# Performance work log

Measured on AMD Instinct MI355X. Metric: run time of the kernel, lower is better.

## Reference

```python
import jax, jax.numpy as jnp
import numpy as np

HIDDEN = 1024
NUM_HEADS = 16
HEAD_DIM = HIDDEN // NUM_HEADS
MASK_BIAS = -10000.0


def setup_inputs() -> dict:
    key = jax.random.key(0)
    ks = jax.random.split(key, 5)
    B, S = 4, 2048
    hidden_states = jax.random.normal(ks[0], (B, S, HIDDEN), dtype=jnp.float32)
    # fused QKV projection (Linear1D_Col): hidden -> 3*hidden
    w_qkv = jax.random.normal(ks[1], (HIDDEN, 3 * HIDDEN), dtype=jnp.float32) * (HIDDEN ** -0.5)
    b_qkv = jax.random.normal(ks[2], (3 * HIDDEN,), dtype=jnp.float32) * 0.02
    # output dense (Linear1D_Row): hidden -> hidden
    w_dense = jax.random.normal(ks[3], (HIDDEN, HIDDEN), dtype=jnp.float32) * (HIDDEN ** -0.5)
    b_dense = jax.random.normal(ks[4], (HIDDEN,), dtype=jnp.float32) * 0.02
    return {"hidden_states": hidden_states, "w_qkv": w_qkv, "b_qkv": b_qkv,
            "w_dense": w_dense, "b_dense": b_dense}


def _split_heads(t):
    # [B, S, H*D] -> [B, H, S, D]
    B, S, _ = t.shape
    return t.reshape(B, S, NUM_HEADS, HEAD_DIM).transpose(0, 2, 1, 3)


def reference(hidden_states, w_qkv, b_qkv, w_dense, b_dense):
    B, S, _ = hidden_states.shape
    kvq = hidden_states @ w_qkv + b_qkv  # [B, S, 3*hidden]
    # NOTE: original chunk order is k, v, q (key first!)
    k, v, q = jnp.split(kvq, 3, axis=-1)
    q = _split_heads(q) * (HEAD_DIM ** -0.5)  # [B, H, S, D]
    k = _split_heads(k)
    v = _split_heads(v)
    scores = jnp.einsum('bhqd,bhkd->bhqk', q, k)  # [B, H, S, S]
    causal = jnp.tril(jnp.ones((S, S), dtype=bool))
    scores = jnp.where(causal[None, None], scores, jnp.asarray(MASK_BIAS, scores.dtype))
    dt = scores.dtype
    attn = jax.nn.softmax(scores.astype(jnp.float32), axis=-1).astype(dt)
    ctx = jnp.einsum('bhqk,bhkd->bhqd', attn, v)  # [B, H, S, D]
    ctx = ctx.transpose(0, 2, 1, 3).reshape(B, S, HIDDEN)
    return ctx @ w_dense + b_dense
```

## Files before the change

kernel.cpp:

```cpp
#include <hip/hip_runtime.h>

#define H_NUM 16
#define HD    64
#define SQ    2048
#define HID   1024
#define MTOK  8192

typedef __attribute__((ext_vector_type(8))) short bf16x8;
typedef __attribute__((ext_vector_type(4))) short s16x4;
typedef __attribute__((ext_vector_type(4))) float f32x4;

__device__ __forceinline__ short f2bf(float f) {
  union { float f; unsigned u; } v; v.f = f;
  unsigned r = v.u + 0x7fffu + ((v.u >> 16) & 1u);
  return (short)(r >> 16);
}

__device__ __forceinline__ float fexp2(float x) {
#if __has_builtin(__builtin_amdgcn_exp2f)
  return __builtin_amdgcn_exp2f(x);
#else
  return exp2f(x);
#endif
}

__device__ __forceinline__ void gload_lds16(const short* g, short* l) {
  __builtin_amdgcn_global_load_lds(
      (const __attribute__((address_space(1))) void*)g,
      (__attribute__((address_space(3))) void*)l, 16, 0, 0);
}

__global__ void k_cvt(const float* __restrict__ in, short* __restrict__ out, int n4) {
  int i = blockIdx.x * blockDim.x + threadIdx.x;
  if (i < n4) {
    float4 f = ((const float4*)in)[i];
    s16x4 o = { f2bf(f.x), f2bf(f.y), f2bf(f.z), f2bf(f.w) };
    ((s16x4*)out)[i] = o;
  }
}

__global__ void k_tr(const float* __restrict__ in, short* __restrict__ out, int R, int C) {
  __shared__ float t[32][33];
  int c0 = blockIdx.x * 32, r0 = blockIdx.y * 32;
  int tx = threadIdx.x, ty = threadIdx.y;
#pragma unroll
  for (int i = 0; i < 4; i++)
    t[ty + 8 * i][tx] = in[(size_t)(r0 + ty + 8 * i) * C + c0 + tx];
  __syncthreads();
#pragma unroll
  for (int i = 0; i < 4; i++)
    out[(size_t)(c0 + ty + 8 * i) * R + r0 + tx] = f2bf(t[tx][ty + 8 * i]);
}

template <int EPI>
__global__ __launch_bounds__(256) void k_gemm(
    const short* __restrict__ A, const short* __restrict__ Bt,
    const float* __restrict__ bias,
    short* __restrict__ qbuf, short* __restrict__ kbuf, short* __restrict__ vtbuf,
    float* __restrict__ outf, int Kd) {
  __shared__ short as[128][64];
  __shared__ short bs[128][64];
  const int tid = threadIdx.x;
  const int w = tid >> 6, l = tid & 63;
  const int lr = l & 15, lk = l >> 4;
  const int wr = w >> 1, wc = w & 1;
  const int nwg = gridDim.x * gridDim.y;
  const int lin = blockIdx.y * gridDim.x + blockIdx.x;
  const int swz = (lin & 7) * (nwg >> 3) + (lin >> 3);
  const int m0 = (swz / gridDim.x) * 128, n0 = (swz % gridDim.x) * 128;

  f32x4 acc[4][4] = {};

  for (int kt = 0; kt < Kd; kt += 64) {
#pragma unroll
    for (int rnd = 0; rnd < 4; ++rnd) {
      int e = rnd * 2048 + w * 512 + l * 8;
      int row = e >> 6, col = e & 63;
      gload_lds16(A + (size_t)(m0 + row) * Kd + kt + col,
                  &as[0][0] + rnd * 2048 + w * 512);
      gload_lds16(Bt + (size_t)(n0 + row) * Kd + kt + col,
                  &bs[0][0] + rnd * 2048 + w * 512);
    }
    __syncthreads();
#pragma unroll
    for (int kk = 0; kk < 2; ++kk) {
      bf16x8 af[4], bf[4];
#pragma unroll
      for (int m = 0; m < 4; ++m)
        af[m] = *(const bf16x8*)&as[wr * 64 + m * 16 + lr][kk * 32 + lk * 8];
#pragma unroll
      for (int n = 0; n < 4; ++n)
        bf[n] = *(const bf16x8*)&bs[wc * 64 + n * 16 + lr][kk * 32 + lk * 8];
      __builtin_amdgcn_s_setprio(1);
#pragma unroll
      for (int m = 0; m < 4; ++m)
#pragma unroll
        for (int n = 0; n < 4; ++n)
          acc[m][n] = __builtin_amdgcn_mfma_f32_16x16x32_bf16(af[m], bf[n], acc[m][n], 0, 0, 0);
      __builtin_amdgcn_s_setprio(0);
    }
    __syncthreads();
  }

  const float SCLQ = 0.125f * 1.44269504088896341f;
#pragma unroll
  for (int n = 0; n < 4; ++n) {
    const int col = n0 + wc * 64 + n * 16 + lr;
    const float bv = bias[col];
    if (EPI == 1) {
#pragma unroll
      for (int m = 0; m < 4; ++m) {
        int row = m0 + wr * 64 + m * 16 + lk * 4;
#pragma unroll
        for (int r = 0; r < 4; ++r)
          outf[(size_t)(row + r) * HID + col] = acc[m][n][r] + bv;
      }
    } else if (col < HID) {
      int h = col >> 6, d = col & 63;
#pragma unroll
      for (int m = 0; m < 4; ++m) {
        int row = m0 + wr * 64 + m * 16 + lk * 4;
        int b = row >> 11, s = row & 2047;
#pragma unroll
        for (int r = 0; r < 4; ++r)
          kbuf[((size_t)(b * H_NUM + h) * SQ + s + r) * HD + d] = f2bf(acc[m][n][r] + bv);
      }
    } else if (col < 2 * HID) {
      int f = col - HID, h = f >> 6, d = f & 63;
#pragma unroll
      for (int m = 0; m < 4; ++m) {
        int row = m0 + wr * 64 + m * 16 + lk * 4;
        int b = row >> 11, s = row & 2047;
        s16x4 pk;
#pragma unroll
        for (int r = 0; r < 4; ++r) pk[r] = f2bf(acc[m][n][r] + bv);
        *(s16x4*)&vtbuf[((size_t)(b * H_NUM + h) * HD + d) * SQ + s] = pk;
      }
    } else {
      int f = col - 2 * HID, h = f >> 6, d = f & 63;
#pragma unroll
      for (int m = 0; m < 4; ++m) {
        int row = m0 + wr * 64 + m * 16 + lk * 4;
        int b = row >> 11, s = row & 2047;
#pragma unroll
        for (int r = 0; r < 4; ++r)
          qbuf[((size_t)(b * H_NUM + h) * SQ + s + r) * HD + d] = f2bf((acc[m][n][r] + bv) * SCLQ);
      }
    }
  }
}

__global__ __launch_bounds__(512) void k_attn(
    const short* __restrict__ Q, const short* __restrict__ K,
    const short* __restrict__ Vt, short* __restrict__ ctx) {
  __shared__ short ks[2][4096];
  __shared__ short vs[2][4096];
  __shared__ short ps[8][16][72];
  const int tid = threadIdx.x;
  const int w = tid >> 6, l = tid & 63;
  const int lr = l & 15, lk = l >> 4;

  const int lin = blockIdx.x;
  const int xcd = lin & 7;
  const int idx = lin >> 3;
  const int qt  = 15 - (idx >> 3);
  const int bh  = xcd * 8 + (idx & 7);
  const int bb = bh >> 4, hh = bh & 15;
  const size_t base = (size_t)bh * (SQ * HD);
  const float THR = 11.5416f;

  const int nt = 2 * qt + 2;
  const int diag = 2 * qt + (w >> 2);
  const int qr = qt * 128 + w * 16;

  const int srow = tid >> 3;
  const int scol = ((tid & 7) * 8) ^ ((srow & 7) * 8);
  const short* kg0 = K + base + srow * HD + scol;
  const short* vg0 = Vt + base + (size_t)srow * SQ + scol;
  short* kld = &ks[0][0] + tid * 8;
  short* vld = &vs[0][0] + tid * 8;
  const int rdswz = (lr & 7) * 8;

  bf16x8 qf[2];
#pragma unroll
  for (int kk = 0; kk < 2; ++kk)
    qf[kk] = *(const bf16x8*)(Q + base + (size_t)(qr + lr) * HD + kk * 32 + lk * 8);

  f32x4 o[4] = {};
  float mrun = -3.0e4f, lsum = 0.f;

  int buf = 0;
  gload_lds16(kg0, kld);
  gload_lds16(vg0, vld);
  __syncthreads();

  for (int t = 0; t < nt; ++t) {
    if (t + 1 < nt) {
      gload_lds16(kg0 + (t + 1) * 4096, kld + (buf ^ 1) * 4096);
      gload_lds16(vg0 + (t + 1) * 64, vld + (buf ^ 1) * 4096);
    }
    if (t <= diag) {
      const short* kb = &ks[buf][0];
      const short* vb = &vs[buf][0];
      f32x4 sf[4] = {};
      __builtin_amdgcn_s_setprio(1);
#pragma unroll
      for (int kk = 0; kk < 2; ++kk)
#pragma unroll
        for (int n = 0; n < 4; ++n) {
          bf16x8 kf = *(const bf16x8*)(kb + (n * 16 + lr) * 64 + ((kk * 32 + lk * 8) ^ rdswz));
          sf[n] = __builtin_amdgcn_mfma_f32_16x16x32_bf16(kf, qf[kk], sf[n], 0, 0, 0);
        }
      __builtin_amdgcn_s_setprio(0);

      if (t == diag) {
        const int qg = qr + lr;
#pragma unroll
        for (int n = 0; n < 4; ++n) {
          int kg = t * 64 + n * 16 + lk * 4;
#pragma unroll
          for (int r = 0; r < 4; ++r)
            if (kg + r > qg) sf[n][r] = -14426.95f;
        }
      }

      float m0 = sf[0][0];
#pragma unroll
      for (int n = 0; n < 4; ++n)
#pragma unroll
        for (int r = 0; r < 4; ++r) m0 = fmaxf(m0, sf[n][r]);
      m0 = fmaxf(m0, __shfl_xor(m0, 16));
      m0 = fmaxf(m0, __shfl_xor(m0, 32));

      if (__any(m0 > mrun + THR)) {
        float mn = fmaxf(mrun, m0);
        float sc = fexp2(mrun - mn);
        float scq[4];
#pragma unroll
        for (int r = 0; r < 4; ++r) scq[r] = __shfl(sc, lk * 4 + r);
#pragma unroll
        for (int nd = 0; nd < 4; ++nd)
#pragma unroll
          for (int r = 0; r < 4; ++r) o[nd][r] *= scq[r];
        lsum *= sc;
        mrun = mn;
      }

      float rs = 0.f;
#pragma unroll
      for (int n = 0; n < 4; ++n) {
        s16x4 pk;
#pragma unroll
        for (int r = 0; r < 4; ++r) {
          float p = fexp2(sf[n][r] - mrun);
          rs += p;
          pk[r] = (short)(__float_as_uint(p) >> 16);
        }
        *(s16x4*)&ps[w][lr][n * 16 + lk * 4] = pk;
      }
      lsum += rs;

      bf16x8 pa[2];
#pragma unroll
      for (int kk = 0; kk < 2; ++kk)
        pa[kk] = *(const bf16x8*)&ps[w][lr][kk * 32 + lk * 8];

      __builtin_amdgcn_s_setprio(1);
#pragma unroll
      for (int kk = 0; kk < 2; ++kk)
#pragma unroll
        for (int nd = 0; nd < 4; ++nd) {
          bf16x8 vf = *(const bf16x8*)(vb + (nd * 16 + lr) * 64 + ((kk * 32 + lk * 8) ^ rdswz));
          o[nd] = __builtin_amdgcn_mfma_f32_16x16x32_bf16(pa[kk], vf, o[nd], 0, 0, 0);
        }
      __builtin_amdgcn_s_setprio(0);
    }
    __syncthreads();
    buf ^= 1;
  }

  lsum += __shfl_xor(lsum, 16);
  lsum += __shfl_xor(lsum, 32);
  float inv = 1.0f / lsum;
  float invq[4];
#pragma unroll
  for (int r = 0; r < 4; ++r) invq[r] = __shfl(inv, lk * 4 + r);
#pragma unroll
  for (int nd = 0; nd < 4; ++nd)
#pragma unroll
    for (int r = 0; r < 4; ++r) {
      int s = qr + lk * 4 + r;
      ctx[((size_t)(bb * SQ + s)) * HID + hh * 64 + nd * 16 + lr] = f2bf(o[nd][r] * invq[r]);
    }
}

extern "C" void kernel_launch(void* const* d_in, const int* in_sizes, int n_in,
                              void* d_out, int out_size, void* d_ws, size_t ws_size,
                              hipStream_t stream) {
  const float* hs   = (const float*)d_in[0];
  const float* wqkv = (const float*)d_in[1];
  const float* bqkv = (const float*)d_in[2];
  const float* wd   = (const float*)d_in[3];
  const float* bd   = (const float*)d_in[4];
  float* out = (float*)d_out;
  char* ws = (char*)d_ws;
  const size_t MB = 1u << 20;

  short* hs_bf  = (short*)(ws);
  short* wqkv_t = (short*)(ws + 16 * MB);
  short* wd_t   = (short*)(ws + 22 * MB);
  short* qbuf   = (short*)(ws + 24 * MB);
  short* kbuf   = (short*)(ws + 40 * MB);
  short* vtbuf  = (short*)(ws + 56 * MB);
  short* ctx    = (short*)(ws + 72 * MB);

  k_cvt<<<8192, 256, 0, stream>>>(hs, hs_bf, MTOK * HID / 4);
  k_tr<<<dim3(96, 32), dim3(32, 8), 0, stream>>>(wqkv, wqkv_t, 1024, 3072);
  k_tr<<<dim3(32, 32), dim3(32, 8), 0, stream>>>(wd, wd_t, 1024, 1024);
  k_gemm<0><<<dim3(24, 64), 256, 0, stream>>>(hs_bf, wqkv_t, bqkv,
                                              qbuf, kbuf, vtbuf, nullptr, 1024);
  k_attn<<<1024, 512, 0, stream>>>(qbuf, kbuf, vtbuf, ctx);
  k_gemm<1><<<dim3(8, 64), 256, 0, stream>>>(ctx, wd_t, bd,
                                             nullptr, nullptr, nullptr, out, 1024);
}
```

Measured before the change: 170.1 us.

## Merge preprocessing kernels and move attention P transpose into register shuffles

Folds the fp32→bf16 conversion of the activations and the two weight transposes into one launch, saving two kernel launches. In the attention kernel, the probability tile is no longer written to and read back from LDS. It is packed with a hardware bf16 pack-convert instruction and rearranged into MFMA A-operand layout with cross-lane shuffles, which removes LDS traffic and the staging buffer. In exchange there are more shuffle instructions per tile, and rounding changes from truncation to round-to-nearest.

```diff
diff --git a/kernel.cpp b/kernel.cpp
--- a/kernel.cpp
+++ b/kernel.cpp
@@ -24,25 +24,41 @@
 #endif
 }
 
+__device__ __forceinline__ int cvt_pk_bf16(float lo, float hi) {
+  int r;
+  asm("v_cvt_pk_bf16_f32 %0, %1, %2" : "=v"(r) : "v"(lo), "v"(hi));
+  return r;
+}
+
 __device__ __forceinline__ void gload_lds16(const short* g, short* l) {
   __builtin_amdgcn_global_load_lds(
       (const __attribute__((address_space(1))) void*)g,
       (__attribute__((address_space(3))) void*)l, 16, 0, 0);
 }
 
-__global__ void k_cvt(const float* __restrict__ in, short* __restrict__ out, int n4) {
-  int i = blockIdx.x * blockDim.x + threadIdx.x;
-  if (i < n4) {
-    float4 f = ((const float4*)in)[i];
+__global__ __launch_bounds__(256) void k_pre(
+    const float* __restrict__ hs, short* __restrict__ hs_bf,
+    const float* __restrict__ wqkv, short* __restrict__ wqkv_t,
+    const float* __restrict__ wd, short* __restrict__ wd_t) {
+  __shared__ float t[32][33];
+  const int b = blockIdx.x, tid = threadIdx.x;
+  if (b < 8192) {
+    int i = b * 256 + tid;
+    float4 f = ((const float4*)hs)[i];
     s16x4 o = { f2bf(f.x), f2bf(f.y), f2bf(f.z), f2bf(f.w) };
-    ((s16x4*)out)[i] = o;
-  }
-}
-
-__global__ void k_tr(const float* __restrict__ in, short* __restrict__ out, int R, int C) {
-  __shared__ float t[32][33];
-  int c0 = blockIdx.x * 32, r0 = blockIdx.y * 32;
-  int tx = threadIdx.x, ty = threadIdx.y;
+    ((s16x4*)hs_bf)[i] = o;
+    return;
+  }
+  const float* in; short* out; int R, C, bx, by;
+  if (b < 8192 + 3072) {
+    int idx = b - 8192; in = wqkv; out = wqkv_t; R = 1024; C = 3072;
+    bx = idx % 96; by = idx / 96;
+  } else {
+    int idx = b - 11264; in = wd; out = wd_t; R = 1024; C = 1024;
+    bx = idx & 31; by = idx >> 5;
+  }
+  const int c0 = bx * 32, r0 = by * 32;
+  const int tx = tid & 31, ty = tid >> 5;
 #pragma unroll
   for (int i = 0; i < 4; i++)
     t[ty + 8 * i][tx] = in[(size_t)(r0 + ty + 8 * i) * C + c0 + tx];
@@ -155,7 +171,6 @@
     const short* __restrict__ Vt, short* __restrict__ ctx) {
   __shared__ short ks[2][4096];
   __shared__ short vs[2][4096];
-  __shared__ short ps[8][16][72];
   const int tid = threadIdx.x;
   const int w = tid >> 6, l = tid & 63;
   const int lr = l & 15, lk = l >> 4;
@@ -189,6 +204,10 @@
   f32x4 o[4] = {};
   float mrun = -3.0e4f, lsum = 0.f;
 
+  const int srcA = lr + ((l & 16) << 1);
+  const int srcB = srcA + 16;
+  const bool hi = (lk >> 1) != 0;
+
   int buf = 0;
   gload_lds16(kg0, kld);
   gload_lds16(vg0, vld);
@@ -246,24 +265,34 @@
         mrun = mn;
       }
 
+      int c[4][2];
       float rs = 0.f;
 #pragma unroll
       for (int n = 0; n < 4; ++n) {
-        s16x4 pk;
-#pragma unroll
-        for (int r = 0; r < 4; ++r) {
-          float p = fexp2(sf[n][r] - mrun);
-          rs += p;
-          pk[r] = (short)(__float_as_uint(p) >> 16);
-        }
-        *(s16x4*)&ps[w][lr][n * 16 + lk * 4] = pk;
+        float p0 = fexp2(sf[n][0] - mrun);
+        float p1 = fexp2(sf[n][1] - mrun);
+        float p2 = fexp2(sf[n][2] - mrun);
+        float p3 = fexp2(sf[n][3] - mrun);
+        rs += (p0 + p1) + (p2 + p3);
+        c[n][0] = cvt_pk_bf16(p0, p1);
+        c[n][1] = cvt_pk_bf16(p2, p3);
       }
       lsum += rs;
 
       bf16x8 pa[2];
 #pragma unroll
-      for (int kk = 0; kk < 2; ++kk)
-        pa[kk] = *(const bf16x8*)&ps[w][lr][kk * 32 + lk * 8];
+      for (int kk = 0; kk < 2; ++kk) {
+        int a0 = __shfl(c[2 * kk][0], srcA), b0 = __shfl(c[2 * kk + 1][0], srcA);
+        int a1 = __shfl(c[2 * kk][1], srcA), b1 = __shfl(c[2 * kk + 1][1], srcA);
+        int a2 = __shfl(c[2 * kk][0], srcB), b2 = __shfl(c[2 * kk + 1][0], srcB);
+        int a3 = __shfl(c[2 * kk][1], srcB), b3 = __shfl(c[2 * kk + 1][1], srcB);
+        union { int d[4]; bf16x8 v; } u;
+        u.d[0] = hi ? b0 : a0;
+        u.d[1] = hi ? b1 : a1;
+        u.d[2] = hi ? b2 : a2;
+        u.d[3] = hi ? b3 : a3;
+        pa[kk] = u.v;
+      }
 
       __builtin_amdgcn_s_setprio(1);
 #pragma unroll
@@ -314,9 +343,7 @@
   short* vtbuf  = (short*)(ws + 56 * MB);
   short* ctx    = (short*)(ws + 72 * MB);
 
-  k_cvt<<<8192, 256, 0, stream>>>(hs, hs_bf, MTOK * HID / 4);
-  k_tr<<<dim3(96, 32), dim3(32, 8), 0, stream>>>(wqkv, wqkv_t, 1024, 3072);
-  k_tr<<<dim3(32, 32), dim3(32, 8), 0, stream>>>(wd, wd_t, 1024, 1024);
+  k_pre<<<12288, 256, 0, stream>>>(hs, hs_bf, wqkv, wqkv_t, wd, wd_t);
   k_gemm<0><<<dim3(24, 64), 256, 0, stream>>>(hs_bf, wqkv_t, bqkv,
                                               qbuf, kbuf, vtbuf, nullptr, 1024);
   k_attn<<<1024, 512, 0, stream>>>(qbuf, kbuf, vtbuf, ctx);
```

Result: slower. 175.1 us (median of 2 runs) (+3.0%).
